# Kernel optimization log

Measured on AMD Instinct MI355X. Metric: run time of the kernel, lower is better.

## Reference

```python
import jax, jax.numpy as jnp
import numpy as np

DN = ('NCDHW', 'OIDHW', 'NCDHW')

def conv3d(x, w):
    return jax.lax.conv_general_dilated(x, w, (1, 1, 1), 'SAME', dimension_numbers=DN)

def maxpool3d(x, win):
    return jax.lax.reduce_window(x, -jnp.inf, jax.lax.max, (1, 1) + win, (1, 1) + win, 'VALID')

def res_block(x, w1, w2, ws):
    # residualBlock3D: conv3x3 -> relu -> conv3x3, 1x1 projection skip when channels change
    y = conv3d(jax.nn.relu(conv3d(x, w1)), w2)
    s = x if ws is None else conv3d(x, ws)
    return jax.nn.relu(y + s)

def cheb_conv(x, edge, W, b):
    # PyG ChebConv, sym norm, lambda_max=2 => scaled Laplacian S = -D^{-1/2} A D^{-1/2}
    # x [B,N,Cin], edge [2,E], W [K,Cin,Cout]
    row, col = edge[0], edge[1]
    N = x.shape[1]
    deg = jnp.zeros((N,), x.dtype).at[row].add(1.0)
    dinv = jnp.where(deg > 0, 1.0 / jnp.sqrt(jnp.maximum(deg, 1.0)), 0.0)
    norm = -(dinv[row] * dinv[col])

    def S(v):  # sparse matvec, batched over B and C
        msg = v[:, row, :] * norm[None, :, None]
        return jnp.zeros_like(v).at[:, col, :].add(msg)

    K = W.shape[0]
    Tx0 = x
    out = jnp.einsum('bnc,cf->bnf', Tx0, W[0])
    if K > 1:
        Tx1 = S(x)
        out = out + jnp.einsum('bnc,cf->bnf', Tx1, W[1])
        for k in range(2, K):
            Tx2 = 2.0 * S(Tx1) - Tx0
            out = out + jnp.einsum('bnc,cf->bnf', Tx2, W[k])
            Tx0, Tx1 = Tx1, Tx2
    if b is not None:
        out = out + b
    return out

def gconv(x, edge, W, b):
    # GConv: ChebConv -> InstanceNorm1d (on [B,N,C]: normalizes over last dim, affine=False) -> relu
    x = cheb_conv(x, edge, W, b)
    mu = x.mean(-1, keepdims=True)
    var = ((x - mu) ** 2).mean(-1, keepdims=True)
    return jax.nn.relu((x - mu) / jnp.sqrt(var + 1e-5))

def grid_sample_3d(feat, pos):
    # feat [B,C,D,H,W]; pos [B,N,3] in [-1,1] with (x->W, y->H, z->D),
    # trilinear, align_corners=True, padding_mode='zeros' (torch F.grid_sample semantics)
    B, C, D, H, W = feat.shape
    gx = (pos[..., 0] + 1.0) * 0.5 * (W - 1)
    gy = (pos[..., 1] + 1.0) * 0.5 * (H - 1)
    gz = (pos[..., 2] + 1.0) * 0.5 * (D - 1)
    x0, y0, z0 = jnp.floor(gx), jnp.floor(gy), jnp.floor(gz)

    def one_batch(fb, gxb, gyb, gzb, x0b, y0b, z0b):
        out = jnp.zeros((C, gxb.shape[0]), fb.dtype)
        for dz in (0, 1):
            for dy in (0, 1):
                for dx in (0, 1):
                    xi, yi, zi = x0b + dx, y0b + dy, z0b + dz
                    w = (1 - jnp.abs(gxb - xi)) * (1 - jnp.abs(gyb - yi)) * (1 - jnp.abs(gzb - zi))
                    valid = (xi >= 0) & (xi <= W - 1) & (yi >= 0) & (yi <= H - 1) & (zi >= 0) & (zi <= D - 1)
                    xc = jnp.clip(xi, 0, W - 1).astype(jnp.int32)
                    yc = jnp.clip(yi, 0, H - 1).astype(jnp.int32)
                    zc = jnp.clip(zi, 0, D - 1).astype(jnp.int32)
                    out = out + fb[:, zc, yc, xc] * (w * valid)[None, :]
        return out

    out = jax.vmap(one_batch)(feat, gx, gy, gz, x0, y0, z0)  # [B,C,N]
    return out.transpose(0, 2, 1)  # [B,N,C]

def igsc(x, W, feat):
    # IGSC_3D with do_skip=True: ChebConv(K=1, no bias) == linear; skip = grid_sample lookup
    pos = jnp.einsum('bnc,cf->bnf', x, W)
    skip = grid_sample_3d(feat, 2.0 * pos - 1.0)
    return jnp.concatenate([x, skip, pos], axis=2), pos

def unpool(x, idx, w):
    # sparse unpooling matmul: 3 nonzeros per output row
    return jnp.einsum('bnkc,nk->bnc', x[:, idx, :], w)

def hybrid_forward(sax, w1_1, w2_1, ws_1, w1_2, w2_2, ws_2, w1_3, w2_3, ws_3,
                   w1_4, w2_4, ws_4, w1_5, w2_5, ws_5, w1_6, w2_6,
                   mu_w, mu_b, sg_w, sg_b, ld_w, ld_b,
                   gc1_w, gc1_b, gc2_w, gc2_b, gc3_w, gc3_b, gc4_w, gc4_b,
                   gc5_w, gc5_b, gcout_w, ig1_w, ig2_w, ig3_w, ig4_w,
                   up_w0, up_w1, up_w2, up_w3,
                   edge0, edge1, edge2, edge3, edge4,
                   up_idx0, up_idx1, up_idx2, up_idx3):
    # ----- Encoder3D -----
    x = res_block(sax, w1_1, w2_1, ws_1); x = maxpool3d(x, (1, 2, 2))
    x = res_block(x, w1_2, w2_2, ws_2);  x = maxpool3d(x, (1, 2, 2))
    l3 = res_block(x, w1_3, w2_3, ws_3); x = maxpool3d(l3, (2, 2, 2))
    l4 = res_block(x, w1_4, w2_4, ws_4); x = maxpool3d(l4, (1, 2, 2))
    l5 = res_block(x, w1_5, w2_5, ws_5); x = maxpool3d(l5, (1, 2, 2))
    l6 = res_block(x, w1_6, w2_6, None)
    # NOTE: original code flattens the PRE-residual6 tensor `x`, not l6 (same shape)
    flat = x.reshape(x.shape[0], -1)
    mu = flat @ mu_w.T + mu_b
    _sigma = flat @ sg_w.T + sg_b  # computed by the module, unused in eval fwd output
    z = mu  # eval mode: z = mu (no sampling)
    # ----- decoder -----
    F5 = gc1_w.shape[1]  # filters[5] = 128
    x = jax.nn.relu(z @ ld_w.T + ld_b).reshape(z.shape[0], -1, F5)  # [B, 688, 128]
    x = gconv(x, edge4, gc1_w, gc1_b)
    x, ds1 = igsc(x, ig1_w, l6)
    x = unpool(x, up_idx3, up_w3)          # 688 -> 1375
    x = gconv(x, edge3, gc2_w, gc2_b)
    x, ds2 = igsc(x, ig2_w, l5)
    x = unpool(x, up_idx2, up_w2)          # 1375 -> 2750
    x = gconv(x, edge2, gc3_w, gc3_b)
    x, ds3 = igsc(x, ig3_w, l4)
    x = unpool(x, up_idx1, up_w1)          # 2750 -> 5500
    x = gconv(x, edge1, gc4_w, gc4_b)
    x, ds4 = igsc(x, ig4_w, l3)
    x = unpool(x, up_idx0, up_w0)          # 5500 -> 11000
    x = gconv(x, edge0, gc5_w, gc5_b)
    x = cheb_conv(x, edge0, gcout_w, None)  # GCout, no bias, no norm
    return x, ds4, ds3, ds2, ds1

def setup_inputs():
    keys = iter(jax.random.split(jax.random.key(0), 128))
    f32 = jnp.float32

    def nrm(shape, fan):
        return jax.random.normal(next(keys), shape, f32) / np.float32(np.sqrt(fan))

    d = {}
    B, S, H, W = 4, 16, 192, 192
    d['sax'] = jax.random.normal(next(keys), (B, 1, S, H, W), f32)
    chans = [1, 8, 16, 32, 64, 128, 128]
    for i in range(1, 7):
        ci, co = chans[i - 1], chans[i]
        d['w1_%d' % i] = nrm((co, ci, 3, 3, 3), ci * 27)
        d['w2_%d' % i] = nrm((co, co, 3, 3, 3), co * 27)
        if i < 6:
            d['ws_%d' % i] = nrm((co, ci, 1, 1, 1), ci)
    flat, lat = 128 * 8 * 6 * 6, 64
    d['mu_w'] = nrm((lat, flat), flat); d['mu_b'] = jnp.zeros((lat,), f32)
    d['sg_w'] = nrm((lat, flat), flat); d['sg_b'] = jnp.zeros((lat,), f32)
    n_nodes = [11000, 5500, 2750, 1375, 688]
    F5, K = 128, 6
    d['ld_w'] = nrm((F5 * n_nodes[-1], lat), lat)
    d['ld_b'] = jnp.zeros((F5 * n_nodes[-1],), f32)
    for i, (ci, co) in enumerate([(128, 64), (195, 64), (195, 32), (99, 32), (67, 32)], 1):
        d['gc%d_w' % i] = nrm((K, ci, co), ci * K)
        d['gc%d_b' % i] = jnp.zeros((co,), f32)
    d['gcout_w'] = nrm((K, 32, 3), 32 * K)
    for i, ci in enumerate([64, 64, 32, 32], 1):
        d['ig%d_w' % i] = nrm((ci, 3), ci)
    for k, N in enumerate(n_nodes):
        d['edge%d' % k] = jax.random.randint(next(keys), (2, 6 * N), 0, N, dtype=jnp.int32)
    for k in range(4):
        No, Ni = n_nodes[k], n_nodes[k + 1]
        d['up_idx%d' % k] = jax.random.randint(next(keys), (No, 3), 0, Ni, dtype=jnp.int32)
        w = jax.random.uniform(next(keys), (No, 3), f32)
        d['up_w%d' % k] = w / w.sum(-1, keepdims=True)
    return d

def reference(sax, w1_1, w2_1, ws_1, w1_2, w2_2, ws_2, w1_3, w2_3, ws_3,
              w1_4, w2_4, ws_4, w1_5, w2_5, ws_5, w1_6, w2_6,
              mu_w, mu_b, sg_w, sg_b, ld_w, ld_b,
              gc1_w, gc1_b, gc2_w, gc2_b, gc3_w, gc3_b, gc4_w, gc4_b,
              gc5_w, gc5_b, gcout_w, ig1_w, ig2_w, ig3_w, ig4_w,
              up_w0, up_w1, up_w2, up_w3,
              edge0, edge1, edge2, edge3, edge4,
              up_idx0, up_idx1, up_idx2, up_idx3):
    return hybrid_forward(sax, w1_1, w2_1, ws_1, w1_2, w2_2, ws_2, w1_3, w2_3, ws_3,
                          w1_4, w2_4, ws_4, w1_5, w2_5, ws_5, w1_6, w2_6,
                          mu_w, mu_b, sg_w, sg_b, ld_w, ld_b,
                          gc1_w, gc1_b, gc2_w, gc2_b, gc3_w, gc3_b, gc4_w, gc4_b,
                          gc5_w, gc5_b, gcout_w, ig1_w, ig2_w, ig3_w, ig4_w,
                          up_w0, up_w1, up_w2, up_w3,
                          edge0, edge1, edge2, edge3, edge4,
                          up_idx0, up_idx1, up_idx2, up_idx3)
```

## Files before the change

kernel.cpp:

```cpp
#include <hip/hip_runtime.h>

typedef long long ll;

#define TPB 256

static inline dim3 gridFor(ll n){ return dim3((unsigned)((n + TPB - 1) / TPB)); }

__global__ void k_copy(const float* __restrict__ in, float* __restrict__ out, ll n){
  ll i = (ll)blockIdx.x*blockDim.x + threadIdx.x;
  if(i<n) out[i] = in[i];
}

template<int COG>
__global__ void k_conv1_t(const float* __restrict__ x, const float* __restrict__ w,
                          float* __restrict__ out, int Ci,int Co,int D,int H,int W)
{
  int HW = H*W, DHW = D*HW;
  int sp = blockIdx.x*blockDim.x + threadIdx.x;
  if(sp>=DHW) return;
  int cg = blockIdx.y, b = blockIdx.z;
  int wv = sp % W, hv = (sp/W) % H, dv = sp / HW;
  ll plane = (ll)DHW;
  const float* xb = x + ((ll)b*Ci)*plane;
  const float* wb = w + ((ll)cg*COG)*Ci*27;
  float acc[COG];
#pragma unroll
  for(int u=0;u<COG;++u) acc[u]=0.f;
  float vd[3],vh[3],vw[3]; int cd[3],ch[3],cw[3];
#pragma unroll
  for(int k=0;k<3;++k){
    int dd=dv+k-1; vd[k]=((unsigned)dd<(unsigned)D)?1.f:0.f; cd[k]=min(max(dd,0),D-1);
    int hh=hv+k-1; vh[k]=((unsigned)hh<(unsigned)H)?1.f:0.f; ch[k]=min(max(hh,0),H-1);
    int ww=wv+k-1; vw[k]=((unsigned)ww<(unsigned)W)?1.f:0.f; cw[k]=min(max(ww,0),W-1);
  }
  for(int ci=0;ci<Ci;++ci){
    const float* xc = xb + (ll)ci*plane;
    float xv[27];
#pragma unroll
    for(int kd=0;kd<3;++kd)
#pragma unroll
      for(int kh=0;kh<3;++kh){
        const float* rowp = xc + ((ll)cd[kd]*H + ch[kh])*W;
        float vdh = vd[kd]*vh[kh];
#pragma unroll
        for(int kw=0;kw<3;++kw)
          xv[(kd*3+kh)*3+kw] = rowp[cw[kw]]*(vdh*vw[kw]);
      }
    const float* wc = wb + ci*27;
#pragma unroll
    for(int u=0;u<COG;++u){
      const float* wu = wc + (ll)u*Ci*27;
      float a = acc[u];
#pragma unroll
      for(int kk=0;kk<27;++kk) a += xv[kk]*wu[kk];
      acc[u]=a;
    }
  }
#pragma unroll
  for(int u=0;u<COG;++u)
    out[((ll)b*Co + cg*COG+u)*plane + sp] = fmaxf(acc[u],0.f);
}

template<int COG>
__global__ void k_conv2res_t(const float* __restrict__ cin, const float* __restrict__ xin,
                             const float* __restrict__ w2, const float* __restrict__ wsk,
                             float* __restrict__ out, int Cm,int Co,int Cs,int D,int H,int W)
{
  int HW = H*W, DHW = D*HW;
  int sp = blockIdx.x*blockDim.x + threadIdx.x;
  if(sp>=DHW) return;
  int cg = blockIdx.y, b = blockIdx.z;
  int wv = sp % W, hv = (sp/W) % H, dv = sp / HW;
  ll plane = (ll)DHW;
  float acc[COG];
  if(wsk){
    const float* xs = xin + ((ll)b*Cs)*plane + sp;
    const float* wr = wsk + (ll)cg*COG*Cs;
#pragma unroll
    for(int u=0;u<COG;++u) acc[u]=0.f;
    for(int cs=0;cs<Cs;++cs){
      float xv = xs[(ll)cs*plane];
#pragma unroll
      for(int u=0;u<COG;++u) acc[u] += xv*wr[(ll)u*Cs+cs];
    }
  } else {
#pragma unroll
    for(int u=0;u<COG;++u) acc[u] = xin[((ll)b*Co + cg*COG+u)*plane + sp];
  }
  float vd[3],vh[3],vw[3]; int cd[3],ch[3],cw[3];
#pragma unroll
  for(int k=0;k<3;++k){
    int dd=dv+k-1; vd[k]=((unsigned)dd<(unsigned)D)?1.f:0.f; cd[k]=min(max(dd,0),D-1);
    int hh=hv+k-1; vh[k]=((unsigned)hh<(unsigned)H)?1.f:0.f; ch[k]=min(max(hh,0),H-1);
    int ww=wv+k-1; vw[k]=((unsigned)ww<(unsigned)W)?1.f:0.f; cw[k]=min(max(ww,0),W-1);
  }
  const float* cb = cin + ((ll)b*Cm)*plane;
  const float* wb = w2 + ((ll)cg*COG)*Cm*27;
  for(int ci=0;ci<Cm;++ci){
    const float* xc = cb + (ll)ci*plane;
    float xv[27];
#pragma unroll
    for(int kd=0;kd<3;++kd)
#pragma unroll
      for(int kh=0;kh<3;++kh){
        const float* rowp = xc + ((ll)cd[kd]*H + ch[kh])*W;
        float vdh = vd[kd]*vh[kh];
#pragma unroll
        for(int kw=0;kw<3;++kw)
          xv[(kd*3+kh)*3+kw] = rowp[cw[kw]]*(vdh*vw[kw]);
      }
    const float* wc = wb + ci*27;
#pragma unroll
    for(int u=0;u<COG;++u){
      const float* wu = wc + (ll)u*Cm*27;
      float a = acc[u];
#pragma unroll
      for(int kk=0;kk<27;++kk) a += xv[kk]*wu[kk];
      acc[u]=a;
    }
  }
#pragma unroll
  for(int u=0;u<COG;++u)
    out[((ll)b*Co + cg*COG+u)*plane + sp] = fmaxf(acc[u],0.f);
}

#define C1_RS 24
template<int COG>
__global__ void k_conv1_lds(const float* __restrict__ x, const float* __restrict__ w,
                            float* __restrict__ out, int Ci,int Co,int D,int H,int W)
{
  const int TO = 16;
  int tilesX = W/TO, tilesY = H/TO;
  int tx = threadIdx.x & 15, ty = threadIdx.x >> 4;
  int bx = blockIdx.x;
  int tX = bx % tilesX; int tmp = bx / tilesX;
  int tY = tmp % tilesY; int dv = tmp / tilesY;
  int cg = blockIdx.y, b = blockIdx.z;
  int oh = tY*TO + ty, ow = tX*TO + tx;
  ll plane = (ll)D*H*W;
  int hbase = tY*TO - 1, wbase = tX*TO - 1;
  __shared__ float lds[3*18*C1_RS];
  float acc[COG];
#pragma unroll
  for(int u=0;u<COG;++u) acc[u]=0.f;
  const float* xb = x + ((ll)b*Ci)*plane;
  const float* wb = w + ((ll)cg*COG)*Ci*27;
  for(int ci=0;ci<Ci;++ci){
    const float* xc = xb + (ll)ci*plane;
    for(int idx=threadIdx.x; idx<3*18*18; idx+=TPB){
      int kd = idx / 324; int rem = idx - kd*324;
      int r = rem / 18, c2 = rem - r*18;
      int dd = dv + kd - 1, hh = hbase + r, ww = wbase + c2;
      float v = 0.f;
      if((unsigned)dd<(unsigned)D && (unsigned)hh<(unsigned)H && (unsigned)ww<(unsigned)W)
        v = xc[((ll)dd*H + hh)*W + ww];
      lds[(kd*18 + r)*C1_RS + c2] = v;
    }
    __syncthreads();
    float xv[27];
#pragma unroll
    for(int kd=0;kd<3;++kd)
#pragma unroll
      for(int kh=0;kh<3;++kh)
#pragma unroll
        for(int kw=0;kw<3;++kw)
          xv[(kd*3+kh)*3+kw] = lds[(kd*18 + (ty+kh))*C1_RS + (tx+kw)];
    const float* wc = wb + ci*27;
#pragma unroll
    for(int u=0;u<COG;++u){
      const float* wu = wc + (ll)u*Ci*27;
      float a = acc[u];
#pragma unroll
      for(int kk=0;kk<27;++kk) a += xv[kk]*wu[kk];
      acc[u]=a;
    }
    __syncthreads();
  }
  ll sp = ((ll)dv*H + oh)*W + ow;
#pragma unroll
  for(int u=0;u<COG;++u)
    out[((ll)b*Co + cg*COG+u)*plane + sp] = fmaxf(acc[u],0.f);
}

template<int COG>
__global__ void k_conv2res_lds(const float* __restrict__ cin, const float* __restrict__ xin,
                               const float* __restrict__ w2, const float* __restrict__ wsk,
                               float* __restrict__ out, int Cm,int Co,int Cs,int D,int H,int W)
{
  const int TO = 16;
  int tilesX = W/TO, tilesY = H/TO;
  int tx = threadIdx.x & 15, ty = threadIdx.x >> 4;
  int bx = blockIdx.x;
  int tX = bx % tilesX; int tmp = bx / tilesX;
  int tY = tmp % tilesY; int dv = tmp / tilesY;
  int cg = blockIdx.y, b = blockIdx.z;
  int oh = tY*TO + ty, ow = tX*TO + tx;
  ll plane = (ll)D*H*W;
  int hbase = tY*TO - 1, wbase = tX*TO - 1;
  __shared__ float lds[3*18*C1_RS];
  ll sp = ((ll)dv*H + oh)*W + ow;
  float acc[COG];
  {
    const float* xs = xin + ((ll)b*Cs)*plane + sp;
    const float* wr = wsk + (ll)cg*COG*Cs;
#pragma unroll
    for(int u=0;u<COG;++u) acc[u]=0.f;
    for(int cs=0;cs<Cs;++cs){
      float xv = xs[(ll)cs*plane];
#pragma unroll
      for(int u=0;u<COG;++u) acc[u] += xv*wr[(ll)u*Cs+cs];
    }
  }
  const float* cb = cin + ((ll)b*Cm)*plane;
  const float* wb = w2 + ((ll)cg*COG)*Cm*27;
  for(int ci=0;ci<Cm;++ci){
    const float* xc = cb + (ll)ci*plane;
    for(int idx=threadIdx.x; idx<3*18*18; idx+=TPB){
      int kd = idx / 324; int rem = idx - kd*324;
      int r = rem / 18, c2 = rem - r*18;
      int dd = dv + kd - 1, hh = hbase + r, ww = wbase + c2;
      float v = 0.f;
      if((unsigned)dd<(unsigned)D && (unsigned)hh<(unsigned)H && (unsigned)ww<(unsigned)W)
        v = xc[((ll)dd*H + hh)*W + ww];
      lds[(kd*18 + r)*C1_RS + c2] = v;
    }
    __syncthreads();
    float xv[27];
#pragma unroll
    for(int kd=0;kd<3;++kd)
#pragma unroll
      for(int kh=0;kh<3;++kh)
#pragma unroll
        for(int kw=0;kw<3;++kw)
          xv[(kd*3+kh)*3+kw] = lds[(kd*18 + (ty+kh))*C1_RS + (tx+kw)];
    const float* wc = wb + ci*27;
#pragma unroll
    for(int u=0;u<COG;++u){
      const float* wu = wc + (ll)u*Cm*27;
      float a = acc[u];
#pragma unroll
      for(int kk=0;kk<27;++kk) a += xv[kk]*wu[kk];
      acc[u]=a;
    }
    __syncthreads();
  }
#pragma unroll
  for(int u=0;u<COG;++u)
    out[((ll)b*Co + cg*COG+u)*plane + sp] = fmaxf(acc[u],0.f);
}

#define CP_RS 36
template<int COG>
__global__ void k_conv2respool_lds(const float* __restrict__ cin, const float* __restrict__ xin,
                                   const float* __restrict__ w2, const float* __restrict__ wsk,
                                   float* __restrict__ out, int Cm,int Co,int Cs,int D,int H,int W)
{
  const int TO = 16;
  int Ho=H/2, Wo=W/2;
  int tilesX = Wo/TO, tilesY = Ho/TO;
  int tx = threadIdx.x & 15, ty = threadIdx.x >> 4;
  int bx = blockIdx.x;
  int tX = bx % tilesX; int tmp = bx / tilesX;
  int tY = tmp % tilesY; int dv = tmp / tilesY;
  int cg = blockIdx.y, b = blockIdx.z;
  int oh = tY*TO + ty, ow = tX*TO + tx;
  ll plane = (ll)D*H*W;
  int hbase = tY*2*TO - 1, wbase = tX*2*TO - 1;
  __shared__ float lds[3*34*CP_RS];

  float acc[COG][4];
#pragma unroll
  for(int u=0;u<COG;++u){
#pragma unroll
    for(int p=0;p<4;++p) acc[u][p]=0.f;
  }
  {
    int hv=2*oh, wv=2*ow;
    ll p00 = ((ll)dv*H + hv)*W + wv;
    const float* xb = xin + ((ll)b*Cs)*plane;
    const float* wr = wsk + (ll)cg*COG*Cs;
    for(int cs=0;cs<Cs;++cs){
      const float* xc = xb + (ll)cs*plane;
      float s00=xc[p00], s01=xc[p00+1], s10=xc[p00+W], s11=xc[p00+W+1];
#pragma unroll
      for(int u=0;u<COG;++u){
        float wv_ = wr[(ll)u*Cs+cs];
        acc[u][0]+=s00*wv_; acc[u][1]+=s01*wv_; acc[u][2]+=s10*wv_; acc[u][3]+=s11*wv_;
      }
    }
  }
  const float* cb = cin + ((ll)b*Cm)*plane;
  const float* wb = w2 + ((ll)cg*COG)*Cm*27;
  for(int ci=0;ci<Cm;++ci){
    const float* xc = cb + (ll)ci*plane;
    for(int idx=threadIdx.x; idx<3*34*34; idx+=TPB){
      int kd = idx / 1156; int rem = idx - kd*1156;
      int r = rem / 34, c2 = rem - r*34;
      int dd = dv + kd - 1, hh = hbase + r, ww = wbase + c2;
      float v = 0.f;
      if((unsigned)dd<(unsigned)D && (unsigned)hh<(unsigned)H && (unsigned)ww<(unsigned)W)
        v = xc[((ll)dd*H + hh)*W + ww];
      int pc = (c2 & 1) ? (17 + (c2>>1)) : (c2>>1);
      lds[(kd*34 + r)*CP_RS + pc] = v;
    }
    __syncthreads();
    float xv[3][4][4];
#pragma unroll
    for(int kd=0;kd<3;++kd)
#pragma unroll
      for(int r=0;r<4;++r){
        int base = (kd*34 + (2*ty+r))*CP_RS;
        xv[kd][r][0] = lds[base + tx];
        xv[kd][r][1] = lds[base + 17 + tx];
        xv[kd][r][2] = lds[base + tx + 1];
        xv[kd][r][3] = lds[base + 18 + tx];
      }
    const float* wc = wb + ci*27;
#pragma unroll
    for(int u=0;u<COG;++u){
      const float* wu = wc + (ll)u*Cm*27;
#pragma unroll
      for(int py=0;py<2;++py)
#pragma unroll
        for(int px=0;px<2;++px){
          float a = acc[u][py*2+px];
#pragma unroll
          for(int kd=0;kd<3;++kd)
#pragma unroll
            for(int kh=0;kh<3;++kh)
#pragma unroll
              for(int kw=0;kw<3;++kw)
                a += xv[kd][py+kh][px+kw]*wu[(kd*3+kh)*3+kw];
          acc[u][py*2+px]=a;
        }
    }
    __syncthreads();
  }
#pragma unroll
  for(int u=0;u<COG;++u){
    float mm = fmaxf(fmaxf(acc[u][0],acc[u][1]),fmaxf(acc[u][2],acc[u][3]));
    out[(((ll)b*Co + cg*COG+u)*D + dv)*(Ho*Wo) + oh*Wo + ow] = fmaxf(mm,0.f);
  }
}

__global__ void k_maxpool(const float* __restrict__ x, float* __restrict__ out,
                          int B,int C,int D,int H,int W,int pd,int ph,int pw)
{
  int Do = D/pd, Ho = H/ph, Wo = W/pw;
  ll total = (ll)B*C*Do*Ho*Wo;
  ll i = (ll)blockIdx.x*blockDim.x + threadIdx.x;
  if(i>=total) return;
  int w0 = (int)(i % Wo); ll t = i / Wo;
  int h0 = (int)(t % Ho); t /= Ho;
  int d0 = (int)(t % Do); t /= Do;
  int c  = (int)(t % C);  int b = (int)(t / C);
  const float* xb = x + ((ll)b*C + c)*D*H*W;
  float m = -3.4e38f;
  for(int dd=0; dd<pd; ++dd)
    for(int hh=0; hh<ph; ++hh)
      for(int ww=0; ww<pw; ++ww){
        float v = xb[(((ll)(d0*pd+dd))*H + (h0*ph+hh))*W + (w0*pw+ww)];
        m = fmaxf(m, v);
      }
  out[i] = m;
}

__global__ void k_linear_red(const float* __restrict__ x, const float* __restrict__ w,
                             const float* __restrict__ bias, float* __restrict__ out,
                             int In, int Out)
{
  int o = blockIdx.x % Out;
  int b = blockIdx.x / Out;
  const float* xr = x + (ll)b*In;
  const float* wr = w + (ll)o*In;
  float s = 0.f;
  for(int i = threadIdx.x; i < In; i += blockDim.x) s += xr[i]*wr[i];
  __shared__ float red[TPB];
  red[threadIdx.x] = s; __syncthreads();
  for(int off = TPB/2; off > 0; off >>= 1){
    if(threadIdx.x < off) red[threadIdx.x] += red[threadIdx.x + off];
    __syncthreads();
  }
  if(threadIdx.x == 0) out[blockIdx.x] = red[0] + bias[o];
}

__global__ void k_ld(const float* __restrict__ z, const float* __restrict__ w,
                     const float* __restrict__ bias, float* __restrict__ out,
                     int B,int Out,int L)
{
  ll i = (ll)blockIdx.x*blockDim.x + threadIdx.x;
  if(i >= (ll)B*Out) return;
  int o = (int)(i % Out); int b = (int)(i / Out);
  const float* zr = z + (ll)b*L;
  const float* wr = w + (ll)o*L;
  float s = bias[o];
  for(int l=0; l<L; ++l) s += zr[l]*wr[l];
  out[i] = fmaxf(s, 0.f);
}

__global__ void k_zero2(float* __restrict__ deg, int* __restrict__ cnt, int N){
  int i = blockIdx.x*blockDim.x + threadIdx.x;
  if(i<N){ deg[i]=0.f; cnt[i]=0; }
}
__global__ void k_degcnt(const int* __restrict__ row, const int* __restrict__ col,
                         float* __restrict__ deg, int* __restrict__ cnt, int E){
  int e = blockIdx.x*blockDim.x + threadIdx.x;
  if(e>=E) return;
  atomicAdd(&deg[row[e]], 1.f);
  atomicAdd(&cnt[col[e]], 1);
}
__global__ void k_scan(const int* __restrict__ cnt, int* __restrict__ rowptr,
                       int* __restrict__ cursor, int N)
{
  __shared__ int ps[TPB];
  int t = threadIdx.x;
  int chunk = (N + TPB - 1)/TPB;
  int s0 = t*chunk, s1 = min(s0+chunk, N);
  int sum = 0;
  for(int i=s0;i<s1;++i) sum += cnt[i];
  ps[t] = sum; __syncthreads();
  for(int off=1; off<TPB; off<<=1){
    int v = (t>=off)? ps[t-off] : 0; __syncthreads();
    ps[t] += v; __syncthreads();
  }
  int base = (t==0)? 0 : ps[t-1];
  for(int i=s0;i<s1;++i){ rowptr[i]=base; cursor[i]=base; base += cnt[i]; }
  if(s1==N) rowptr[N]=base;
}
__global__ void k_fill(const int* __restrict__ row, const int* __restrict__ col,
                       const float* __restrict__ deg, int* __restrict__ cursor,
                       int* __restrict__ src, float* __restrict__ wgt, int E)
{
  int e = blockIdx.x*blockDim.x + threadIdx.x;
  if(e>=E) return;
  int r = row[e], c = col[e];
  float dr = deg[r], dc = deg[c];
  float ir = dr > 0.f ? rsqrtf(dr) : 0.f;
  float ic = dc > 0.f ? rsqrtf(dc) : 0.f;
  int pos = atomicAdd(&cursor[c], 1);
  src[pos] = r;
  wgt[pos] = -(ir*ic);
}

template<int G>
__global__ void k_cheb_hop(const float* __restrict__ v, const float* __restrict__ t0,
                           const int* __restrict__ rowptr, const int* __restrict__ src,
                           const float* __restrict__ cw, const float* __restrict__ Wk,
                           float* __restrict__ t2, float* __restrict__ xout,
                           int B,int N,int Ci,int Co,int mode)
{
  extern __shared__ float lds[];
  ll g0 = (ll)blockIdx.x*G;
  ll BN = (ll)B*N;
  int tot = G*Ci;
  for(int idx=threadIdx.x; idx<tot; idx+=blockDim.x){
    int g = idx / Ci, c = idx - g*Ci;
    ll bj = g0 + g;
    float s = 0.f;
    if(bj < BN){
      if(mode==0){
        s = v[bj*(ll)Ci + c];
      } else {
        int b = (int)(bj / N), j = (int)(bj - (ll)b*N);
        int e0 = rowptr[j], e1 = rowptr[j+1];
        const float* vb = v + (ll)b*N*Ci;
        for(int e=e0;e<e1;++e) s += vb[(ll)src[e]*Ci + c]*cw[e];
        if(mode==2) s = 2.f*s - t0[bj*(ll)Ci + c];
        t2[bj*(ll)Ci + c] = s;
      }
    }
    lds[idx] = s;
  }
  __syncthreads();
  int totB = G*Co;
  for(int idx=threadIdx.x; idx<totB; idx+=blockDim.x){
    int g = idx / Co, co = idx - g*Co;
    ll bj = g0 + g;
    if(bj >= BN) continue;
    const float* tr = lds + g*Ci;
    float s = 0.f;
    for(int c=0;c<Ci;++c) s += tr[c]*Wk[(ll)c*Co + co];
    if(mode==0) xout[bj*(ll)Co+co] = s;
    else xout[bj*(ll)Co+co] += s;
  }
}

__global__ void k_inorm(float* __restrict__ x, const float* __restrict__ bias, ll BN, int C)
{
  ll r = (ll)blockIdx.x*blockDim.x + threadIdx.x;
  if(r>=BN) return;
  float* xr = x + r*(ll)C;
  float mu = 0.f;
  for(int c=0;c<C;++c){ float v = xr[c] + bias[c]; xr[c]=v; mu += v; }
  mu /= (float)C;
  float var = 0.f;
  for(int c=0;c<C;++c){ float d = xr[c]-mu; var += d*d; }
  var /= (float)C;
  float inv = rsqrtf(var + 1e-5f);
  for(int c=0;c<C;++c) xr[c] = fmaxf((xr[c]-mu)*inv, 0.f);
}

__global__ void k_copycols(const float* __restrict__ x, float* __restrict__ cat,
                           ll BN, int Cx, int Ctot)
{
  ll i = (ll)blockIdx.x*blockDim.x + threadIdx.x;
  if(i >= BN*(ll)Cx) return;
  int c = (int)(i % Cx); ll r = i / Cx;
  cat[r*(ll)Ctot + c] = x[i];
}
__global__ void k_pos(const float* __restrict__ x, const float* __restrict__ igw,
                      float* __restrict__ cat, float* __restrict__ ds,
                      ll BN, int Cx, int Ctot, int posoff)
{
  ll i = (ll)blockIdx.x*blockDim.x + threadIdx.x;
  if(i>=BN) return;
  const float* xr = x + i*(ll)Cx;
  float p0=0.f,p1=0.f,p2=0.f;
  for(int c=0;c<Cx;++c){
    float v = xr[c];
    p0 += v*igw[c*3+0];
    p1 += v*igw[c*3+1];
    p2 += v*igw[c*3+2];
  }
  float* rowp = cat + i*(ll)Ctot + posoff;
  rowp[0]=p0; rowp[1]=p1; rowp[2]=p2;
  ds[i*3+0]=p0; ds[i*3+1]=p1; ds[i*3+2]=p2;
}
__global__ void k_gsample(const float* __restrict__ feat, float* __restrict__ cat,
                          int B,int N,int Cf,int D,int H,int W,int Ctot,int xoff,int posoff)
{
  ll i = (ll)blockIdx.x*blockDim.x + threadIdx.x;
  ll total = (ll)B*N*Cf;
  if(i>=total) return;
  int c = (int)(i % Cf); ll t = i / Cf;
  int n = (int)(t % N); int b = (int)(t / N);
  float* rowp = cat + ((ll)b*N + n)*Ctot;
  float px = rowp[posoff+0], py = rowp[posoff+1], pz = rowp[posoff+2];
  float gx = (2.f*px - 1.f + 1.f)*0.5f*(W-1);
  float gy = (2.f*py - 1.f + 1.f)*0.5f*(H-1);
  float gz = (2.f*pz - 1.f + 1.f)*0.5f*(D-1);
  float x0 = floorf(gx), y0 = floorf(gy), z0 = floorf(gz);
  const float* fb = feat + ((ll)b*Cf + c)*D*H*W;
  float acc = 0.f;
  for(int dz=0; dz<2; ++dz)
    for(int dy=0; dy<2; ++dy)
      for(int dx=0; dx<2; ++dx){
        float xi = x0+dx, yi = y0+dy, zi = z0+dz;
        float wgt = (1.f-fabsf(gx-xi))*(1.f-fabsf(gy-yi))*(1.f-fabsf(gz-zi));
        bool valid = (xi>=0.f)&&(xi<=(float)(W-1))&&(yi>=0.f)&&(yi<=(float)(H-1))&&(zi>=0.f)&&(zi<=(float)(D-1));
        int xc = min(max((int)xi,0),W-1);
        int yc = min(max((int)yi,0),H-1);
        int zc = min(max((int)zi,0),D-1);
        if(valid) acc += fb[((ll)zc*H + yc)*W + xc]*wgt;
      }
  rowp[xoff + c] = acc;
}

__global__ void k_unpool(const float* __restrict__ xin, const int* __restrict__ idx,
                         const float* __restrict__ w, float* __restrict__ out,
                         int B,int Ni,int No,int C)
{
  ll i = (ll)blockIdx.x*blockDim.x + threadIdx.x;
  ll total = (ll)B*No*C;
  if(i>=total) return;
  int c = (int)(i % C); ll t = i / C;
  int no = (int)(t % No); int b = (int)(t / No);
  float s = 0.f;
  for(int k=0;k<3;++k){
    s += xin[((ll)b*Ni + idx[no*3+k])*C + c]*w[no*3+k];
  }
  out[i] = s;
}

static const ll BO_A   = 0;
static const ll BO_B   = 75497472;
static const ll BO_C   = 94371840;
static const ll BO_L3  = 103809024;
static const ll BO_L4  = 122683392;
static const ll BO_L5  = 127401984;
static const ll BO_L6  = 129761280;
static const ll BO_P5  = 130940928;
static const ll BO_Z   = 132120576;
static const ll BO_DX   = 0;
static const ll BO_DT1  = 11792000;
static const ll BO_DT2  = 23584000;
static const ll BO_DO   = 35376000;
static const ll BO_DCAT = 41008000;
static const ll BO_DDEG = 46904000;
static const ll BO_CNT  = 46948096;
static const ll BO_RP   = 46992128;
static const ll BO_CUR  = 47036160;
static const ll BO_SRC  = 47080192;
static const ll BO_CW   = 47344256;

extern "C" void kernel_launch(void* const* d_in, const int* in_sizes, int n_in,
                              void* d_out, int out_size, void* d_ws, size_t ws_size,
                              hipStream_t stream)
{
  (void)in_sizes; (void)n_in; (void)out_size; (void)ws_size;
  const int B = 4;
  const float* sax = (const float*)d_in[0];
  const float *w1[7], *w2[7], *wsk[7];
  for(int i=1;i<=5;++i){
    w1[i]  = (const float*)d_in[1 + (i-1)*3];
    w2[i]  = (const float*)d_in[2 + (i-1)*3];
    wsk[i] = (const float*)d_in[3 + (i-1)*3];
  }
  w1[6] = (const float*)d_in[16]; w2[6] = (const float*)d_in[17]; wsk[6] = nullptr;
  const float* mu_w = (const float*)d_in[18];
  const float* mu_b = (const float*)d_in[19];
  const float* ld_w = (const float*)d_in[22];
  const float* ld_b = (const float*)d_in[23];
  const float *gcw[5], *gcb[5];
  for(int i=0;i<5;++i){ gcw[i] = (const float*)d_in[24+2*i]; gcb[i] = (const float*)d_in[25+2*i]; }
  const float* gcout_w = (const float*)d_in[34];
  const float* igw[4];
  for(int i=0;i<4;++i) igw[i] = (const float*)d_in[35+i];
  const int* edge[5];
  for(int i=0;i<5;++i) edge[i] = (const int*)d_in[39+i];
  const int* upidx[4]; const float* upw[4];
  for(int i=0;i<4;++i){ upidx[i] = (const int*)d_in[44+2*i]; upw[i] = (const float*)d_in[45+2*i]; }
  float* out = (float*)d_out;
  char* base = (char*)d_ws;

  float* A  = (float*)(base + BO_A);
  float* Bb = (float*)(base + BO_B);
  float* Cb = (float*)(base + BO_C);
  float* L3 = (float*)(base + BO_L3);
  float* L4 = (float*)(base + BO_L4);
  float* L5 = (float*)(base + BO_L5);
  float* L6 = (float*)(base + BO_L6);
  float* P5 = (float*)(base + BO_P5);
  float* Z  = (float*)(base + BO_Z);
  float* DX  = (float*)(base + BO_DX);
  float* DT1 = (float*)(base + BO_DT1);
  float* DT2 = (float*)(base + BO_DT2);
  float* DO_ = (float*)(base + BO_DO);
  float* DCAT= (float*)(base + BO_DCAT);
  float* DDEG= (float*)(base + BO_DDEG);
  int*   CNT = (int*)(base + BO_CNT);
  int*   RP  = (int*)(base + BO_RP);
  int*   CUR = (int*)(base + BO_CUR);
  int*   SRC = (int*)(base + BO_SRC);
  float* CW  = (float*)(base + BO_CW);

  auto convgrid = [&](int DHW, int Co, int COG){ return dim3((unsigned)((DHW+TPB-1)/TPB), Co/COG, B); };
  auto tilegrid = [&](int D,int H,int W,int Co,int COG){
    return dim3((unsigned)((H/16)*(W/16)*D), Co/COG, B);
  };

  k_conv1_lds<8><<<tilegrid(16,192,192,8,8),TPB,0,stream>>>(sax, w1[1], A, 1,8,16,192,192);
  k_conv2respool_lds<8><<<tilegrid(16,96,96,8,8),TPB,0,stream>>>(A, sax, w2[1], wsk[1], Bb, 8,8,1,16,192,192);
  k_conv1_lds<16><<<tilegrid(16,96,96,16,16),TPB,0,stream>>>(Bb, w1[2], A, 8,16,16,96,96);
  k_conv2respool_lds<8><<<tilegrid(16,48,48,16,8),TPB,0,stream>>>(A, Bb, w2[2], wsk[2], Cb, 16,16,8,16,96,96);
  k_conv1_lds<16><<<tilegrid(16,48,48,32,16),TPB,0,stream>>>(Cb, w1[3], A, 16,32,16,48,48);
  k_conv2res_lds<16><<<tilegrid(16,48,48,32,16),TPB,0,stream>>>(A, Cb, w2[3], wsk[3], L3, 32,32,16,16,48,48);
  { ll np=(ll)B*32*8*24*24;
    k_maxpool<<<gridFor(np),TPB,0,stream>>>(L3, Bb, B,32,16,48,48,2,2,2); }
  k_conv1_t<4><<<convgrid(8*24*24,64,4),TPB,0,stream>>>(Bb, w1[4], A, 32,64,8,24,24);
  k_conv2res_t<4><<<convgrid(8*24*24,64,4),TPB,0,stream>>>(A, Bb, w2[4], wsk[4], L4, 64,64,32,8,24,24);
  { ll np=(ll)B*64*8*12*12;
    k_maxpool<<<gridFor(np),TPB,0,stream>>>(L4, Cb, B,64,8,24,24,1,2,2); }
  k_conv1_t<4><<<convgrid(8*12*12,128,4),TPB,0,stream>>>(Cb, w1[5], A, 64,128,8,12,12);
  k_conv2res_t<4><<<convgrid(8*12*12,128,4),TPB,0,stream>>>(A, Cb, w2[5], wsk[5], L5, 128,128,64,8,12,12);
  { ll np=(ll)B*128*8*6*6;
    k_maxpool<<<gridFor(np),TPB,0,stream>>>(L5, P5, B,128,8,12,12,1,2,2); }
  k_conv1_t<2><<<convgrid(8*6*6,128,2),TPB,0,stream>>>(P5, w1[6], A, 128,128,8,6,6);
  k_conv2res_t<2><<<convgrid(8*6*6,128,2),TPB,0,stream>>>(A, P5, w2[6], nullptr, L6, 128,128,128,8,6,6);

  k_linear_red<<<dim3(B*64),TPB,0,stream>>>(P5, mu_w, mu_b, Z, 36864, 64);
  k_ld<<<gridFor((ll)B*88064),TPB,0,stream>>>(Z, ld_w, ld_b, DX, B, 88064, 64);

  auto build_csr = [&](const int* e, int N, int E){
    const int* row = e; const int* col = e + E;
    k_zero2<<<gridFor(N),TPB,0,stream>>>(DDEG, CNT, N);
    k_degcnt<<<gridFor(E),TPB,0,stream>>>(row, col, DDEG, CNT, E);
    k_scan<<<1,TPB,0,stream>>>(CNT, RP, CUR, N);
    k_fill<<<gridFor(E),TPB,0,stream>>>(row, col, DDEG, CUR, SRC, CW, E);
  };

  const int G = 4;
  auto cheb = [&](float* xin, float* t1, float* t2, float* xout,
                  const int* e, int N, int E, const float* Wg, int Ci, int Co, bool build){
    if(build) build_csr(e, N, E);
    ll BN = (ll)B*N;
    unsigned nb = (unsigned)((BN + G - 1)/G);
    size_t shm = (size_t)G*Ci*sizeof(float);
    k_cheb_hop<G><<<nb,TPB,shm,stream>>>(xin, nullptr, RP, SRC, CW, Wg, nullptr, xout, B,N,Ci,Co, 0);
    k_cheb_hop<G><<<nb,TPB,shm,stream>>>(xin, nullptr, RP, SRC, CW, Wg+(ll)Ci*Co, t1, xout, B,N,Ci,Co, 1);
    float *b0=xin, *b1=t1, *b2=t2;
    for(int k=2;k<6;++k){
      k_cheb_hop<G><<<nb,TPB,shm,stream>>>(b1, b0, RP, SRC, CW, Wg+(ll)k*Ci*Co, b2, xout, B,N,Ci,Co, 2);
      float* tmp=b0; b0=b1; b1=b2; b2=tmp;
    }
  };

  auto igsc = [&](float* x, float* cat, const float* ig, const float* feat,
                  int N, int Cx, int Cf, int D,int Hh,int Ww, float* ds){
    int Ctot = Cx + Cf + 3;
    ll BN = (ll)B*N;
    k_copycols<<<gridFor(BN*Cx),TPB,0,stream>>>(x, cat, BN, Cx, Ctot);
    k_pos<<<gridFor(BN),TPB,0,stream>>>(x, ig, cat, ds, BN, Cx, Ctot, Cx+Cf);
    k_gsample<<<gridFor(BN*(ll)Cf),TPB,0,stream>>>(feat, cat, B,N,Cf,D,Hh,Ww,Ctot,Cx,Cx+Cf);
  };

  float* out_x  = out;
  float* out_d4 = out + 132000;
  float* out_d3 = out + 198000;
  float* out_d2 = out + 231000;
  float* out_d1 = out + 247500;

  cheb(DX, DT1, DT2, DO_, edge[4], 688, 4128, gcw[0], 128, 64, true);
  k_inorm<<<gridFor((ll)B*688),TPB,0,stream>>>(DO_, gcb[0], (ll)B*688, 64);
  igsc(DO_, DCAT, igw[0], L6, 688, 64, 128, 8,6,6, out_d1);
  k_unpool<<<gridFor((ll)B*1375*195),TPB,0,stream>>>(DCAT, upidx[3], upw[3], DX, B, 688, 1375, 195);

  cheb(DX, DT1, DT2, DO_, edge[3], 1375, 8250, gcw[1], 195, 64, true);
  k_inorm<<<gridFor((ll)B*1375),TPB,0,stream>>>(DO_, gcb[1], (ll)B*1375, 64);
  igsc(DO_, DCAT, igw[1], L5, 1375, 64, 128, 8,12,12, out_d2);
  k_unpool<<<gridFor((ll)B*2750*195),TPB,0,stream>>>(DCAT, upidx[2], upw[2], DX, B, 1375, 2750, 195);

  cheb(DX, DT1, DT2, DO_, edge[2], 2750, 16500, gcw[2], 195, 32, true);
  k_inorm<<<gridFor((ll)B*2750),TPB,0,stream>>>(DO_, gcb[2], (ll)B*2750, 32);
  igsc(DO_, DCAT, igw[2], L4, 2750, 32, 64, 8,24,24, out_d3);
  k_unpool<<<gridFor((ll)B*5500*99),TPB,0,stream>>>(DCAT, upidx[1], upw[1], DX, B, 2750, 5500, 99);

  cheb(DX, DT1, DT2, DO_, edge[1], 5500, 33000, gcw[3], 99, 32, true);
  k_inorm<<<gridFor((ll)B*5500),TPB,0,stream>>>(DO_, gcb[3], (ll)B*5500, 32);
  igsc(DO_, DCAT, igw[3], L3, 5500, 32, 32, 16,48,48, out_d4);
  k_unpool<<<gridFor((ll)B*11000*67),TPB,0,stream>>>(DCAT, upidx[0], upw[0], DX, B, 5500, 11000, 67);

  cheb(DX, DT1, DT2, DO_, edge[0], 11000, 66000, gcw[4], 67, 32, true);
  k_inorm<<<gridFor((ll)B*11000),TPB,0,stream>>>(DO_, gcb[4], (ll)B*11000, 32);

  cheb(DO_, DT1, DT2, DCAT, edge[0], 11000, 66000, gcout_w, 32, 3, false);
  k_copy<<<gridFor(132000LL),TPB,0,stream>>>(DCAT, out_x, 132000LL);
}
```

Measured before the change: 3.882 ms.

## Batch CSR builds for all graph levels and fuse small GCN launches

Builds the CSR for all five mesh graphs up front in one set of batched kernels (zero, degree count, scan, fill), indexed by blockIdx.y and an offsets struct, instead of four launches per level. It merges the copy-columns and position-projection kernels into one launch and writes the final ChebConv output straight into the output buffer, which drops the trailing copy kernel. It also undoes the padded, parity-split LDS layout in the pooled conv2 kernel and goes back to a plain 34-wide layout, which may bring back LDS bank conflicts. The point is to cut kernel launch count and serial tiny kernels, at the cost of relying on a hardcoded E = 6N edge count for every graph.

```diff
diff --git a/kernel.cpp b/kernel.cpp
--- a/kernel.cpp
+++ b/kernel.cpp
@@ -5,11 +5,6 @@
 #define TPB 256
 
 static inline dim3 gridFor(ll n){ return dim3((unsigned)((n + TPB - 1) / TPB)); }
-
-__global__ void k_copy(const float* __restrict__ in, float* __restrict__ out, ll n){
-  ll i = (ll)blockIdx.x*blockDim.x + threadIdx.x;
-  if(i<n) out[i] = in[i];
-}
 
 template<int COG>
 __global__ void k_conv1_t(const float* __restrict__ x, const float* __restrict__ w,
@@ -249,7 +244,6 @@
     out[((ll)b*Co + cg*COG+u)*plane + sp] = fmaxf(acc[u],0.f);
 }
 
-#define CP_RS 36
 template<int COG>
 __global__ void k_conv2respool_lds(const float* __restrict__ cin, const float* __restrict__ xin,
                                    const float* __restrict__ w2, const float* __restrict__ wsk,
@@ -266,7 +260,7 @@
   int oh = tY*TO + ty, ow = tX*TO + tx;
   ll plane = (ll)D*H*W;
   int hbase = tY*2*TO - 1, wbase = tX*2*TO - 1;
-  __shared__ float lds[3*34*CP_RS];
+  __shared__ float lds[3*34*34];
 
   float acc[COG][4];
 #pragma unroll
@@ -300,21 +294,17 @@
       float v = 0.f;
       if((unsigned)dd<(unsigned)D && (unsigned)hh<(unsigned)H && (unsigned)ww<(unsigned)W)
         v = xc[((ll)dd*H + hh)*W + ww];
-      int pc = (c2 & 1) ? (17 + (c2>>1)) : (c2>>1);
-      lds[(kd*34 + r)*CP_RS + pc] = v;
+      lds[idx] = v;
     }
     __syncthreads();
     float xv[3][4][4];
 #pragma unroll
     for(int kd=0;kd<3;++kd)
 #pragma unroll
-      for(int r=0;r<4;++r){
-        int base = (kd*34 + (2*ty+r))*CP_RS;
-        xv[kd][r][0] = lds[base + tx];
-        xv[kd][r][1] = lds[base + 17 + tx];
-        xv[kd][r][2] = lds[base + tx + 1];
-        xv[kd][r][3] = lds[base + 18 + tx];
-      }
+      for(int r=0;r<4;++r)
+#pragma unroll
+        for(int j=0;j<4;++j)
+          xv[kd][r][j] = lds[(kd*34 + (2*ty+r))*34 + (2*tx+j)];
     const float* wc = wb + ci*27;
 #pragma unroll
     for(int u=0;u<COG;++u){
@@ -398,48 +388,58 @@
   out[i] = fmaxf(s, 0.f);
 }
 
-__global__ void k_zero2(float* __restrict__ deg, int* __restrict__ cnt, int N){
+struct CsrOffs { int N[5]; int nOff[5]; int rpOff[5]; int eOff[5]; };
+
+__global__ void k_csr_zero(float* __restrict__ deg, int* __restrict__ cnt, int tot){
   int i = blockIdx.x*blockDim.x + threadIdx.x;
-  if(i<N){ deg[i]=0.f; cnt[i]=0; }
-}
-__global__ void k_degcnt(const int* __restrict__ row, const int* __restrict__ col,
-                         float* __restrict__ deg, int* __restrict__ cnt, int E){
+  if(i<tot){ deg[i]=0.f; cnt[i]=0; }
+}
+__global__ void k_csr_degcnt(const int* e0,const int* e1,const int* e2,const int* e3,const int* e4,
+                             CsrOffs o, float* __restrict__ deg, int* __restrict__ cnt){
+  int g = blockIdx.y;
+  int E = 6*o.N[g];
   int e = blockIdx.x*blockDim.x + threadIdx.x;
   if(e>=E) return;
-  atomicAdd(&deg[row[e]], 1.f);
-  atomicAdd(&cnt[col[e]], 1);
-}
-__global__ void k_scan(const int* __restrict__ cnt, int* __restrict__ rowptr,
-                       int* __restrict__ cursor, int N)
-{
+  const int* eg = (g==0)?e0:(g==1)?e1:(g==2)?e2:(g==3)?e3:e4;
+  int nb = o.nOff[g];
+  atomicAdd(&deg[nb+eg[e]], 1.f);
+  atomicAdd(&cnt[nb+eg[E+e]], 1);
+}
+__global__ void k_csr_scan(CsrOffs o, const int* __restrict__ cnt,
+                           int* __restrict__ rp, int* __restrict__ cur){
+  int g = blockIdx.x;
+  int N = o.N[g]; int nb = o.nOff[g]; int rb = o.rpOff[g];
   __shared__ int ps[TPB];
   int t = threadIdx.x;
   int chunk = (N + TPB - 1)/TPB;
   int s0 = t*chunk, s1 = min(s0+chunk, N);
   int sum = 0;
-  for(int i=s0;i<s1;++i) sum += cnt[i];
+  for(int i=s0;i<s1;++i) sum += cnt[nb+i];
   ps[t] = sum; __syncthreads();
   for(int off=1; off<TPB; off<<=1){
     int v = (t>=off)? ps[t-off] : 0; __syncthreads();
     ps[t] += v; __syncthreads();
   }
   int base = (t==0)? 0 : ps[t-1];
-  for(int i=s0;i<s1;++i){ rowptr[i]=base; cursor[i]=base; base += cnt[i]; }
-  if(s1==N) rowptr[N]=base;
-}
-__global__ void k_fill(const int* __restrict__ row, const int* __restrict__ col,
-                       const float* __restrict__ deg, int* __restrict__ cursor,
-                       int* __restrict__ src, float* __restrict__ wgt, int E)
-{
+  for(int i=s0;i<s1;++i){ rp[rb+i]=base; cur[nb+i]=base; base += cnt[nb+i]; }
+  if(s1==N) rp[rb+N]=base;
+}
+__global__ void k_csr_fill(const int* e0,const int* e1,const int* e2,const int* e3,const int* e4,
+                           CsrOffs o, const float* __restrict__ deg, int* __restrict__ cur,
+                           int* __restrict__ src, float* __restrict__ cw){
+  int g = blockIdx.y;
+  int E = 6*o.N[g];
   int e = blockIdx.x*blockDim.x + threadIdx.x;
   if(e>=E) return;
-  int r = row[e], c = col[e];
-  float dr = deg[r], dc = deg[c];
+  const int* eg = (g==0)?e0:(g==1)?e1:(g==2)?e2:(g==3)?e3:e4;
+  int nb = o.nOff[g], eb = o.eOff[g];
+  int r = eg[e], c = eg[E+e];
+  float dr = deg[nb+r], dc = deg[nb+c];
   float ir = dr > 0.f ? rsqrtf(dr) : 0.f;
   float ic = dc > 0.f ? rsqrtf(dc) : 0.f;
-  int pos = atomicAdd(&cursor[c], 1);
-  src[pos] = r;
-  wgt[pos] = -(ir*ic);
+  int pos = atomicAdd(&cur[nb+c], 1);
+  src[eb+pos] = r;
+  cw[eb+pos] = -(ir*ic);
 }
 
 template<int G>
@@ -500,31 +500,24 @@
   for(int c=0;c<C;++c) xr[c] = fmaxf((xr[c]-mu)*inv, 0.f);
 }
 
-__global__ void k_copycols(const float* __restrict__ x, float* __restrict__ cat,
-                           ll BN, int Cx, int Ctot)
+__global__ void k_igsc_pre(const float* __restrict__ x, const float* __restrict__ igw,
+                           float* __restrict__ cat, float* __restrict__ ds,
+                           ll BN, int Cx, int Ctot, int posoff)
 {
   ll i = (ll)blockIdx.x*blockDim.x + threadIdx.x;
-  if(i >= BN*(ll)Cx) return;
-  int c = (int)(i % Cx); ll r = i / Cx;
-  cat[r*(ll)Ctot + c] = x[i];
-}
-__global__ void k_pos(const float* __restrict__ x, const float* __restrict__ igw,
-                      float* __restrict__ cat, float* __restrict__ ds,
-                      ll BN, int Cx, int Ctot, int posoff)
-{
-  ll i = (ll)blockIdx.x*blockDim.x + threadIdx.x;
-  if(i>=BN) return;
-  const float* xr = x + i*(ll)Cx;
-  float p0=0.f,p1=0.f,p2=0.f;
-  for(int c=0;c<Cx;++c){
-    float v = xr[c];
-    p0 += v*igw[c*3+0];
-    p1 += v*igw[c*3+1];
-    p2 += v*igw[c*3+2];
-  }
-  float* rowp = cat + i*(ll)Ctot + posoff;
-  rowp[0]=p0; rowp[1]=p1; rowp[2]=p2;
-  ds[i*3+0]=p0; ds[i*3+1]=p1; ds[i*3+2]=p2;
+  ll tot = BN*(ll)(Cx+3);
+  if(i>=tot) return;
+  int c = (int)(i % (Cx+3)); ll r = i / (Cx+3);
+  if(c < Cx){
+    cat[r*(ll)Ctot + c] = x[r*(ll)Cx + c];
+  } else {
+    int p = c - Cx;
+    const float* xr = x + r*(ll)Cx;
+    float s = 0.f;
+    for(int cc=0;cc<Cx;++cc) s += xr[cc]*igw[cc*3+p];
+    cat[r*(ll)Ctot + posoff + p] = s;
+    ds[r*3+p] = s;
+  }
 }
 __global__ void k_gsample(const float* __restrict__ feat, float* __restrict__ cat,
                           int B,int N,int Cf,int D,int H,int W,int Ctot,int xoff,int posoff)
@@ -587,11 +580,11 @@
 static const ll BO_DO   = 35376000;
 static const ll BO_DCAT = 41008000;
 static const ll BO_DDEG = 46904000;
-static const ll BO_CNT  = 46948096;
-static const ll BO_RP   = 46992128;
-static const ll BO_CUR  = 47036160;
-static const ll BO_SRC  = 47080192;
-static const ll BO_CW   = 47344256;
+static const ll BO_CNT  = 46989504;
+static const ll BO_RP   = 47075008;
+static const ll BO_CUR  = 47160512;
+static const ll BO_SRC  = 47246016;
+static const ll BO_CW   = 47757632;
 
 extern "C" void kernel_launch(void* const* d_in, const int* in_sizes, int n_in,
                               void* d_out, int out_size, void* d_ws, size_t ws_size,
@@ -671,26 +664,35 @@
   k_linear_red<<<dim3(B*64),TPB,0,stream>>>(P5, mu_w, mu_b, Z, 36864, 64);
   k_ld<<<gridFor((ll)B*88064),TPB,0,stream>>>(Z, ld_w, ld_b, DX, B, 88064, 64);
 
-  auto build_csr = [&](const int* e, int N, int E){
-    const int* row = e; const int* col = e + E;
-    k_zero2<<<gridFor(N),TPB,0,stream>>>(DDEG, CNT, N);
-    k_degcnt<<<gridFor(E),TPB,0,stream>>>(row, col, DDEG, CNT, E);
-    k_scan<<<1,TPB,0,stream>>>(CNT, RP, CUR, N);
-    k_fill<<<gridFor(E),TPB,0,stream>>>(row, col, DDEG, CUR, SRC, CW, E);
-  };
+  CsrOffs offs;
+  { int N_[5]={11000,5500,2750,1375,688};
+    int no=0, eo=0;
+    for(int g=0; g<5; ++g){
+      offs.N[g]=N_[g]; offs.nOff[g]=no; offs.rpOff[g]=no+g; offs.eOff[g]=eo;
+      no += N_[g]; eo += 6*N_[g];
+    } }
+  const int TOTN = 21313, MAXE = 66000;
+  k_csr_zero<<<gridFor(TOTN),TPB,0,stream>>>(DDEG, CNT, TOTN);
+  { dim3 g((unsigned)((MAXE+TPB-1)/TPB), 5);
+    k_csr_degcnt<<<g,TPB,0,stream>>>(edge[0],edge[1],edge[2],edge[3],edge[4], offs, DDEG, CNT);
+    k_csr_scan<<<dim3(5),TPB,0,stream>>>(offs, CNT, RP, CUR);
+    k_csr_fill<<<g,TPB,0,stream>>>(edge[0],edge[1],edge[2],edge[3],edge[4], offs, DDEG, CUR, SRC, CW); }
 
   const int G = 4;
   auto cheb = [&](float* xin, float* t1, float* t2, float* xout,
-                  const int* e, int N, int E, const float* Wg, int Ci, int Co, bool build){
-    if(build) build_csr(e, N, E);
+                  int gi, const float* Wg, int Ci, int Co){
+    int N = offs.N[gi];
+    const int* RPg = RP + offs.rpOff[gi];
+    const int* SRCg = SRC + offs.eOff[gi];
+    const float* CWg = CW + offs.eOff[gi];
     ll BN = (ll)B*N;
     unsigned nb = (unsigned)((BN + G - 1)/G);
     size_t shm = (size_t)G*Ci*sizeof(float);
-    k_cheb_hop<G><<<nb,TPB,shm,stream>>>(xin, nullptr, RP, SRC, CW, Wg, nullptr, xout, B,N,Ci,Co, 0);
-    k_cheb_hop<G><<<nb,TPB,shm,stream>>>(xin, nullptr, RP, SRC, CW, Wg+(ll)Ci*Co, t1, xout, B,N,Ci,Co, 1);
+    k_cheb_hop<G><<<nb,TPB,shm,stream>>>(xin, nullptr, RPg, SRCg, CWg, Wg, nullptr, xout, B,N,Ci,Co, 0);
+    k_cheb_hop<G><<<nb,TPB,shm,stream>>>(xin, nullptr, RPg, SRCg, CWg, Wg+(ll)Ci*Co, t1, xout, B,N,Ci,Co, 1);
     float *b0=xin, *b1=t1, *b2=t2;
     for(int k=2;k<6;++k){
-      k_cheb_hop<G><<<nb,TPB,shm,stream>>>(b1, b0, RP, SRC, CW, Wg+(ll)k*Ci*Co, b2, xout, B,N,Ci,Co, 2);
+      k_cheb_hop<G><<<nb,TPB,shm,stream>>>(b1, b0, RPg, SRCg, CWg, Wg+(ll)k*Ci*Co, b2, xout, B,N,Ci,Co, 2);
       float* tmp=b0; b0=b1; b1=b2; b2=tmp;
     }
   };
@@ -699,8 +701,7 @@
                   int N, int Cx, int Cf, int D,int Hh,int Ww, float* ds){
     int Ctot = Cx + Cf + 3;
     ll BN = (ll)B*N;
-    k_copycols<<<gridFor(BN*Cx),TPB,0,stream>>>(x, cat, BN, Cx, Ctot);
-    k_pos<<<gridFor(BN),TPB,0,stream>>>(x, ig, cat, ds, BN, Cx, Ctot, Cx+Cf);
+    k_igsc_pre<<<gridFor(BN*(ll)(Cx+3)),TPB,0,stream>>>(x, ig, cat, ds, BN, Cx, Ctot, Cx+Cf);
     k_gsample<<<gridFor(BN*(ll)Cf),TPB,0,stream>>>(feat, cat, B,N,Cf,D,Hh,Ww,Ctot,Cx,Cx+Cf);
   };
 
@@ -710,29 +711,28 @@
   float* out_d2 = out + 231000;
   float* out_d1 = out + 247500;
 
-  cheb(DX, DT1, DT2, DO_, edge[4], 688, 4128, gcw[0], 128, 64, true);
+  cheb(DX, DT1, DT2, DO_, 4, gcw[0], 128, 64);
   k_inorm<<<gridFor((ll)B*688),TPB,0,stream>>>(DO_, gcb[0], (ll)B*688, 64);
   igsc(DO_, DCAT, igw[0], L6, 688, 64, 128, 8,6,6, out_d1);
   k_unpool<<<gridFor((ll)B*1375*195),TPB,0,stream>>>(DCAT, upidx[3], upw[3], DX, B, 688, 1375, 195);
 
-  cheb(DX, DT1, DT2, DO_, edge[3], 1375, 8250, gcw[1], 195, 64, true);
+  cheb(DX, DT1, DT2, DO_, 3, gcw[1], 195, 64);
   k_inorm<<<gridFor((ll)B*1375),TPB,0,stream>>>(DO_, gcb[1], (ll)B*1375, 64);
   igsc(DO_, DCAT, igw[1], L5, 1375, 64, 128, 8,12,12, out_d2);
   k_unpool<<<gridFor((ll)B*2750*195),TPB,0,stream>>>(DCAT, upidx[2], upw[2], DX, B, 1375, 2750, 195);
 
-  cheb(DX, DT1, DT2, DO_, edge[2], 2750, 16500, gcw[2], 195, 32, true);
+  cheb(DX, DT1, DT2, DO_, 2, gcw[2], 195, 32);
   k_inorm<<<gridFor((ll)B*2750),TPB,0,stream>>>(DO_, gcb[2], (ll)B*2750, 32);
   igsc(DO_, DCAT, igw[2], L4, 2750, 32, 64, 8,24,24, out_d3);
   k_unpool<<<gridFor((ll)B*5500*99),TPB,0,stream>>>(DCAT, upidx[1], upw[1], DX, B, 2750, 5500, 99);
 
-  cheb(DX, DT1, DT2, DO_, edge[1], 5500, 33000, gcw[3], 99, 32, true);
+  cheb(DX, DT1, DT2, DO_, 1, gcw[3], 99, 32);
   k_inorm<<<gridFor((ll)B*5500),TPB,0,stream>>>(DO_, gcb[3], (ll)B*5500, 32);
   igsc(DO_, DCAT, igw[3], L3, 5500, 32, 32, 16,48,48, out_d4);
   k_unpool<<<gridFor((ll)B*11000*67),TPB,0,stream>>>(DCAT, upidx[0], upw[0], DX, B, 5500, 11000, 67);
 
-  cheb(DX, DT1, DT2, DO_, edge[0], 11000, 66000, gcw[4], 67, 32, true);
+  cheb(DX, DT1, DT2, DO_, 0, gcw[4], 67, 32);
   k_inorm<<<gridFor((ll)B*11000),TPB,0,stream>>>(DO_, gcb[4], (ll)B*11000, 32);
 
-  cheb(DO_, DT1, DT2, DCAT, edge[0], 11000, 66000, gcout_w, 32, 3, false);
-  k_copy<<<gridFor(132000LL),TPB,0,stream>>>(DCAT, out_x, 132000LL);
-}
+  cheb(DO_, DT1, DT2, out_x, 0, gcout_w, 32, 3);
+}
```

After: 3.793 ms. -2.3%, faster.
